# Performance work log

Measured on AMD Instinct MI355X. Metric: run time of the kernel, lower is better.

## Reference

```python
import jax, jax.numpy as jnp
import numpy as np

B, S, H, D = 1, 2048, 24, 128   # batch, img seq, heads, head_dim
RD = 64                          # rotary_emb_dim (partial RoPE)
IPS, IPD = 512, 1152             # ip tokens, ip feature dim
HID = H * D                      # 3072
EPS = 1e-6


def _heads(x):
    # (B, S, H*D) -> (B, H, S, D)
    b, s, _ = x.shape
    return x.reshape(b, s, H, D).transpose(0, 2, 1, 3)


def _rmsnorm(x, scale):
    # RMSNorm with p<0 path: rms = ||x||_2 / sqrt(D); y = scale * x / (rms + eps)
    rms = jnp.linalg.norm(x, axis=-1, keepdims=True) * (D ** -0.5)
    return scale * (x / (rms + EPS))


def _rope(x, sin, cos):
    # rotate-half RoPE on first RD channels, pass-through on the rest
    xr, xp = x[..., :RD], x[..., RD:]
    x1, x2 = jnp.split(xr, 2, axis=-1)
    rot = jnp.concatenate([-x2, x1], axis=-1)
    return jnp.concatenate([xr * cos + rot * sin, xp], axis=-1)


def setup_inputs() -> dict:
    key = jax.random.key(0)
    ks = jax.random.split(key, 16)
    std = 0.02
    inp = {
        "hidden_states": jax.random.normal(ks[0], (B, S, HID), jnp.float32),
        "ip_hidden_states": jax.random.normal(ks[1], (B, IPS, IPD), jnp.float32),
        "sin": jax.random.normal(ks[2], (S, RD), jnp.float32),
        "cos": jax.random.normal(ks[3], (S, RD), jnp.float32),
        "Wq": jax.random.normal(ks[4], (HID, HID), jnp.float32) * std,
        "bq": jnp.zeros((HID,), jnp.float32),
        "Wk": jax.random.normal(ks[5], (HID, HID), jnp.float32) * std,
        "bk": jnp.zeros((HID,), jnp.float32),
        "Wv": jax.random.normal(ks[6], (HID, HID), jnp.float32) * std,
        "bv": jnp.zeros((HID,), jnp.float32),
        "Wo": jax.random.normal(ks[7], (HID, HID), jnp.float32) * std,
        "bo": jnp.zeros((HID,), jnp.float32),
        "Wk_ip": jax.random.normal(ks[8], (HID, IPD), jnp.float32) * std,
        "bk_ip": jnp.zeros((HID,), jnp.float32),
        "Wv_ip": jax.random.normal(ks[9], (HID, IPD), jnp.float32) * std,
        "bv_ip": jnp.zeros((HID,), jnp.float32),
        "q_scale": jnp.ones((D,), jnp.float32),
        "k_scale": jnp.ones((D,), jnp.float32),
    }
    return inp


def reference(hidden_states, ip_hidden_states, sin, cos,
              Wq, bq, Wk, bk, Wv, bv, Wo, bo,
              Wk_ip, bk_ip, Wv_ip, bv_ip, q_scale, k_scale):
    scale = 1.0  # default `scale` kwarg
    # projections (self-attention: encoder_hidden_states = hidden_states)
    q = _heads(hidden_states @ Wq.T + bq)        # (B,H,S,D)
    k = _heads(hidden_states @ Wk.T + bk)
    v = _heads(hidden_states @ Wv.T + bv)
    k_ip = _heads(ip_hidden_states @ Wk_ip.T + bk_ip)   # (B,H,IPS,D)
    v_ip = _heads(ip_hidden_states @ Wv_ip.T + bv_ip)

    # IP branch uses RMS-normed, head_dim^-0.5-scaled, UNROTATED q and k_ip
    # (key_ip is rotated in the source but the rotated value is never used)
    q_norm = _rmsnorm(q, q_scale) * (D ** -0.5)
    k_ip_norm = _rmsnorm(k_ip, k_scale) * (D ** -0.5)

    # main branch: RoPE'd q/k, raw dot product (alpha=1.0, no 1/sqrt(d))
    q_rot = _rope(q, sin, cos)
    k_rot = _rope(k, sin, cos)

    scores = jnp.einsum('bhsd,bhtd->bhst', q_rot, k_rot)
    probs = jax.nn.softmax(scores, axis=-1)
    scores_ip = scale * jnp.einsum('bhsd,bhtd->bhst', q_norm, k_ip_norm)
    probs_ip = jax.nn.softmax(scores_ip, axis=-1)

    out = jnp.einsum('bhst,bhtd->bhsd', probs, v) \
        + jnp.einsum('bhst,bhtd->bhsd', probs_ip, v_ip)
    out = out.transpose(0, 2, 1, 3).reshape(B, S, HID)  # batch_to_head_dim
    out = out @ Wo.T + bo                                # to_out[0]; dropout = id
    return out
```

## Files before the change

kernel.cpp:

```cpp
#include <hip/hip_runtime.h>
#include <stdint.h>

#define S_LEN 2048
#define NH    24
#define HD    128
#define HID   3072
#define IPS   512
#define IPD   1152

using f16   = __fp16;
using f16x4 = __fp16 __attribute__((ext_vector_type(4)));
using f16x8 = __fp16 __attribute__((ext_vector_type(8)));
using f32x4 = float  __attribute__((ext_vector_type(4)));
using f32x16 = float __attribute__((ext_vector_type(16)));

__device__ __forceinline__ void glds16(const f16* g, f16* l) {
  __builtin_amdgcn_global_load_lds((const __attribute__((address_space(1))) void*)g,
                                   (__attribute__((address_space(3))) void*)l,
                                   16, 0, 0);
}

struct CastArgs { const float* src[8]; f16* dst[8]; long n4[8]; };

__global__ void k_cvt_all(CastArgs a, long total4) {
  long i = blockIdx.x * 256L + threadIdx.x;
  if (i >= total4) return;
  long r = i; int s = 0;
  while (r >= a.n4[s]) { r -= a.n4[s]; s++; }
  float4 v = ((const float4*)a.src[s])[r];
  f16x4 o;
  o.x = (f16)v.x; o.y = (f16)v.y; o.z = (f16)v.z; o.w = (f16)v.w;
  ((f16x4*)a.dst[s])[r] = o;
}

__global__ __launch_bounds__(256) void k_gemm_nt(
    const f16* __restrict__ A,
    const f16* __restrict__ B0, const f16* __restrict__ B1, const f16* __restrict__ B2,
    const float* __restrict__ bias0, const float* __restrict__ bias1, const float* __restrict__ bias2,
    void* __restrict__ C0, void* __restrict__ C1, void* __restrict__ C2,
    int M, int N, int K, int out_f32)
{
  const int z = blockIdx.z;
  const f16*   B    = (z == 0) ? B0 : (z == 1) ? B1 : B2;
  const float* bias = (z == 0) ? bias0 : (z == 1) ? bias1 : bias2;
  void*        Cv   = (z == 0) ? C0 : (z == 1) ? C1 : C2;

  __shared__ f16 As[128 * 64];
  __shared__ f16 Bs[128 * 64];

  const int tid = threadIdx.x;
  const int w   = tid >> 6, l = tid & 63;
  const int l31 = l & 31, hi = l >> 5;
  const int bm = blockIdx.y * 128, bn = blockIdx.x * 128;
  const int wm = (w >> 1) * 64,    wn = (w & 1) * 64;

  f32x16 acc[2][2] = {};

  const int r0   = w * 32;
  const int srow = l >> 3;
  const int gch  = (l & 7) ^ (srow & 7);
  const f16* Ag = A + (long)(bm + r0 + srow) * K + gch * 8;
  const f16* Bg = B + (long)(bn + r0 + srow) * K + gch * 8;
  f16* lA = &As[r0 * 64];
  f16* lB = &Bs[r0 * 64];
  const long rs8 = 8L * K;

  const int swz = l & 7;

  for (int k0 = 0; k0 < K; k0 += 64) {
#pragma unroll
    for (int g = 0; g < 4; g++) {
      glds16(Ag + g * rs8 + k0, lA + g * 512);
      glds16(Bg + g * rs8 + k0, lB + g * 512);
    }
    __syncthreads();

#pragma unroll
    for (int ks = 0; ks < 4; ks++) {
      const int pos = ((ks * 2 + hi) ^ swz) * 8;
      f16x8 af[2], bf[2];
#pragma unroll
      for (int mi = 0; mi < 2; mi++)
        af[mi] = *(const f16x8*)&As[(wm + mi * 32 + l31) * 64 + pos];
#pragma unroll
      for (int nj = 0; nj < 2; nj++)
        bf[nj] = *(const f16x8*)&Bs[(wn + nj * 32 + l31) * 64 + pos];
#pragma unroll
      for (int mi = 0; mi < 2; mi++)
#pragma unroll
        for (int nj = 0; nj < 2; nj++)
          acc[mi][nj] = __builtin_amdgcn_mfma_f32_32x32x16_f16(af[mi], bf[nj], acc[mi][nj], 0, 0, 0);
    }
    __syncthreads();
  }

#pragma unroll
  for (int mi = 0; mi < 2; mi++)
#pragma unroll
    for (int nj = 0; nj < 2; nj++) {
      const int col = bn + wn + nj * 32 + l31;
      const float bvv = bias[col];
      const int rowb = bm + wm + mi * 32 + 4 * hi;
#pragma unroll
      for (int reg = 0; reg < 16; reg++) {
        const int row = rowb + (reg & 3) + 8 * (reg >> 2);
        float v = acc[mi][nj][reg] + bvv;
        if (out_f32) ((float*)Cv)[(long)row * N + col] = v;
        else         ((f16*)Cv)[(long)row * N + col] = (f16)v;
      }
    }
}

__global__ void k_qprep(const f16* __restrict__ x, const float* __restrict__ snp,
                        const float* __restrict__ csp, const float* __restrict__ scale,
                        f16* __restrict__ qrot, f16* __restrict__ qnorm, int rows) {
  int gw = (blockIdx.x * 256 + threadIdx.x) >> 6;
  int l  = threadIdx.x & 63;
  if (gw >= rows) return;
  long base = (long)gw * HD;
  int s = gw / NH;
  int d = 2 * l;
  float a = (float)x[base + d];
  float b = (float)x[base + d + 1];

  float ss = a * a + b * b;
#pragma unroll
  for (int off = 32; off >= 1; off >>= 1) ss += __shfl_xor(ss, off, 64);
  float rms = sqrtf(ss * (1.0f / HD));
  float inv = 0.08838834764831845f / (rms + 1e-6f);
  qnorm[base + d]     = (f16)(a * scale[d] * inv);
  qnorm[base + d + 1] = (f16)(b * scale[d + 1] * inv);

  float pa = __shfl_xor(a, 16, 64);
  float pb = __shfl_xor(b, 16, 64);
  float ra, rb;
  if (d < 64) {
    float sgn = (d < 32) ? -1.0f : 1.0f;
    ra = a * csp[s * 64 + d]     + sgn * pa * snp[s * 64 + d];
    rb = b * csp[s * 64 + d + 1] + sgn * pb * snp[s * 64 + d + 1];
  } else {
    ra = a; rb = b;
  }
  qrot[base + d]     = (f16)ra;
  qrot[base + d + 1] = (f16)rb;
}

__global__ void k_krope_pack(const f16* __restrict__ src, const float* __restrict__ snp,
                             const float* __restrict__ csp, f16* __restrict__ dst,
                             int T, int nchunk) {
  int i = blockIdx.x * 256 + threadIdx.x;
  if (i >= nchunk) return;
  int d8 = i % 384;
  int t  = i / 384;
  int h  = d8 >> 4;
  int d  = (d8 & 15) * 8;
  f16x8 x = *(const f16x8*)(src + (long)i * 8);
  f16x8 o;
  if (d < 64) {
    f16x8 p = (d < 32) ? *(const f16x8*)(src + (long)i * 8 + 32)
                       : *(const f16x8*)(src + (long)i * 8 - 32);
    float sgn = (d < 32) ? -1.0f : 1.0f;
#pragma unroll
    for (int j = 0; j < 8; j++) {
      float cs = csp[t * 64 + d + j], sn = snp[t * 64 + d + j];
      o[j] = (f16)((float)x[j] * cs + sgn * (float)p[j] * sn);
    }
  } else {
    o = x;
  }
  long off = ((((long)h * (T >> 4) + (t >> 4)) * 4 + (d >> 5)) * 64 + ((d >> 3) & 3) * 16 + (t & 15)) * 8;
  *(f16x8*)(dst + off) = o;
}

__global__ void k_rms_pack(const f16* __restrict__ x, const float* __restrict__ scale,
                           f16* __restrict__ dst, int T, int rows) {
  int gw  = (blockIdx.x * 256 + threadIdx.x) >> 6;
  int l   = threadIdx.x & 63;
  int sub = l >> 4, l16 = l & 15;
  int row = gw * 4 + sub;
  if (row >= rows) return;
  int t = row / NH, h = row - t * NH;
  int d = l16 * 8;
  f16x8 v = *(const f16x8*)(x + (long)row * HD + d);
  float ss = 0.f;
#pragma unroll
  for (int j = 0; j < 8; j++) { float f = (float)v[j]; ss += f * f; }
  ss += __shfl_xor(ss, 1, 64);
  ss += __shfl_xor(ss, 2, 64);
  ss += __shfl_xor(ss, 4, 64);
  ss += __shfl_xor(ss, 8, 64);
  float rms = sqrtf(ss * (1.0f / HD));
  float inv = 0.08838834764831845f / (rms + 1e-6f);
  f16x8 o;
#pragma unroll
  for (int j = 0; j < 8; j++) o[j] = (f16)((float)v[j] * scale[d + j] * inv);
  long off = ((((long)h * (T >> 4) + (t >> 4)) * 4 + (d >> 5)) * 64 + ((d >> 3) & 3) * 16 + (t & 15)) * 8;
  *(f16x8*)(dst + off) = o;
}

__global__ __launch_bounds__(256) void k_vpack(const f16* __restrict__ v, f16* __restrict__ dst, int T) {
  __shared__ f16 Ts[128 * 72];
  int h = blockIdx.y, tb = blockIdx.x, t0 = tb * 64;
  int tid = threadIdx.x;
  int r = tid >> 2, c4 = tid & 3;
#pragma unroll
  for (int cc = 0; cc < 4; cc++) {
    int ch = c4 * 4 + cc;
    f16x8 x = *(const f16x8*)(v + (long)(t0 + r) * HID + h * HD + ch * 8);
#pragma unroll
    for (int j = 0; j < 8; j++)
      Ts[(ch * 8 + j) * 72 + r] = x[j];
  }
  __syncthreads();
  int l16 = tid & 15, jd = (tid >> 4) & 7, ks = tid >> 7;
#pragma unroll
  for (int quad = 0; quad < 4; quad++) {
    f16x8 x = *(const f16x8*)&Ts[(jd * 16 + l16) * 72 + ks * 32 + quad * 8];
    long off = ((((long)h * (T >> 6) + tb) * 2 + ks) * 8 + jd) * 512 + (quad * 16 + l16) * 8;
    *(f16x8*)(dst + off) = x;
  }
}

__global__ __launch_bounds__(256) void k_flash2(
    const f16* __restrict__ Q, const f16* __restrict__ Kp, const f16* __restrict__ Vp,
    f16* __restrict__ Opart, long part_stride, float2* __restrict__ ml, int p0,
    int T, int Tc)
{
  __shared__ f16 Ps[4][32 * 72];

  const int h    = blockIdx.y;
  const int sp   = blockIdx.z;
  const int tid  = threadIdx.x, w = tid >> 6, l = tid & 63;
  const int quad = l >> 4, l16 = l & 15;
  const int qr   = blockIdx.x * 128 + w * 32;
  const int Tt16 = T >> 4, Tt64 = T >> 6;

  f16x8 qf[2][4];
#pragma unroll
  for (int mt = 0; mt < 2; mt++)
#pragma unroll
    for (int kq = 0; kq < 4; kq++)
      qf[mt][kq] = *(const f16x8*)(Q + (long)(qr + mt * 16 + l16) * HID + h * HD + kq * 32 + quad * 8);

  f32x4 o[2][8] = {};
  float m_run[8], l_run[8];
#pragma unroll
  for (int i = 0; i < 8; i++) { m_run[i] = -1e30f; l_run[i] = 0.f; }

  f16* myP = &Ps[w][0];
  const int t_begin = sp * Tc, t_end = t_begin + Tc;

  for (int t0 = t_begin; t0 < t_end; t0 += 64) {
    f32x4 s[2][4] = {};
#pragma unroll
    for (int kq = 0; kq < 4; kq++) {
      f16x8 kf[4];
#pragma unroll
      for (int jn = 0; jn < 4; jn++)
        kf[jn] = *(const f16x8*)(Kp + (((long)(h * Tt16 + (t0 >> 4) + jn) * 4 + kq) * 64 + l) * 8);
#pragma unroll
      for (int mt = 0; mt < 2; mt++)
#pragma unroll
        for (int jn = 0; jn < 4; jn++)
          s[mt][jn] = __builtin_amdgcn_mfma_f32_16x16x32_f16(qf[mt][kq], kf[jn], s[mt][jn], 0, 0, 0);
    }

#pragma unroll
    for (int mt = 0; mt < 2; mt++) {
#pragma unroll
      for (int r = 0; r < 4; r++) {
        float mx = fmaxf(fmaxf(s[mt][0][r], s[mt][1][r]), fmaxf(s[mt][2][r], s[mt][3][r]));
        mx = fmaxf(mx, __shfl_xor(mx, 1, 64));
        mx = fmaxf(mx, __shfl_xor(mx, 2, 64));
        mx = fmaxf(mx, __shfl_xor(mx, 4, 64));
        mx = fmaxf(mx, __shfl_xor(mx, 8, 64));
        const int ri = mt * 4 + r;
        float mn = fmaxf(m_run[ri], mx);
        float al = __expf(m_run[ri] - mn);
        m_run[ri] = mn;
        float p0v = __expf(s[mt][0][r] - mn);
        float p1v = __expf(s[mt][1][r] - mn);
        float p2v = __expf(s[mt][2][r] - mn);
        float p3v = __expf(s[mt][3][r] - mn);
        s[mt][0][r] = p0v; s[mt][1][r] = p1v; s[mt][2][r] = p2v; s[mt][3][r] = p3v;
        l_run[ri] = l_run[ri] * al + (p0v + p1v + p2v + p3v);
#pragma unroll
        for (int jd = 0; jd < 8; jd++) o[mt][jd][r] *= al;
      }
    }

#pragma unroll
    for (int mt = 0; mt < 2; mt++)
#pragma unroll
      for (int jn = 0; jn < 4; jn++)
#pragma unroll
        for (int r = 0; r < 4; r++)
          myP[(mt * 16 + quad * 4 + r) * 72 + jn * 16 + l16] = (f16)s[mt][jn][r];

#pragma unroll
    for (int ks = 0; ks < 2; ks++) {
      f16x8 pf[2];
#pragma unroll
      for (int mt = 0; mt < 2; mt++)
        pf[mt] = *(const f16x8*)&myP[(mt * 16 + l16) * 72 + ks * 32 + quad * 8];
      f16x8 vf[8];
#pragma unroll
      for (int jd = 0; jd < 8; jd++)
        vf[jd] = *(const f16x8*)(Vp + ((((long)(h * Tt64 + (t0 >> 6)) * 2 + ks) * 8 + jd) * 64 + l) * 8);
#pragma unroll
      for (int jd = 0; jd < 8; jd++)
#pragma unroll
        for (int mt = 0; mt < 2; mt++)
          o[mt][jd] = __builtin_amdgcn_mfma_f32_16x16x32_f16(pf[mt], vf[jd], o[mt][jd], 0, 0, 0);
    }
  }

#pragma unroll
  for (int i = 0; i < 8; i++) {
    float v = l_run[i];
    v += __shfl_xor(v, 1, 64);
    v += __shfl_xor(v, 2, 64);
    v += __shfl_xor(v, 4, 64);
    v += __shfl_xor(v, 8, 64);
    l_run[i] = v;
  }

  f16* Od = Opart + (long)sp * part_stride;
#pragma unroll
  for (int mt = 0; mt < 2; mt++)
#pragma unroll
    for (int jd = 0; jd < 8; jd++)
#pragma unroll
      for (int r = 0; r < 4; r++) {
        int row = qr + mt * 16 + quad * 4 + r;
        int col = h * HD + jd * 16 + l16;
        Od[(long)row * HID + col] = (f16)o[mt][jd][r];
      }
  if (l16 == 0) {
#pragma unroll
    for (int mt = 0; mt < 2; mt++)
#pragma unroll
      for (int r = 0; r < 4; r++) {
        int row = qr + mt * 16 + quad * 4 + r;
        float2 v; v.x = m_run[mt * 4 + r]; v.y = l_run[mt * 4 + r];
        ml[((long)(p0 + sp) * NH + h) * S_LEN + row] = v;
      }
  }
}

__global__ void k_combine(const f16* __restrict__ O0, const f16* __restrict__ O1,
                          const f16* __restrict__ O2, const f16* __restrict__ O3,
                          const f16* __restrict__ O4, const f16* __restrict__ O5,
                          const float2* __restrict__ ml, f16* __restrict__ out, int nchunk) {
  int i = blockIdx.x * 256 + threadIdx.x;
  if (i >= nchunk) return;
  int s = i / 384, d8 = i - s * 384, h = d8 >> 4;
  long base = (long)h * S_LEN + s;
  float2 a0 = ml[0 * NH * S_LEN + base];
  float2 a1 = ml[1L * NH * S_LEN + base];
  float2 a2 = ml[2L * NH * S_LEN + base];
  float2 a3 = ml[3L * NH * S_LEN + base];
  float2 a4 = ml[4L * NH * S_LEN + base];
  float2 a5 = ml[5L * NH * S_LEN + base];
  float M1 = fmaxf(fmaxf(a0.x, a1.x), fmaxf(a2.x, a3.x));
  float e0 = __expf(a0.x - M1), e1 = __expf(a1.x - M1), e2 = __expf(a2.x - M1), e3 = __expf(a3.x - M1);
  float L1 = a0.y * e0 + a1.y * e1 + a2.y * e2 + a3.y * e3;
  float w0 = e0 / L1, w1 = e1 / L1, w2 = e2 / L1, w3 = e3 / L1;
  float M2 = fmaxf(a4.x, a5.x);
  float e4 = __expf(a4.x - M2), e5 = __expf(a5.x - M2);
  float L2 = a4.y * e4 + a5.y * e5;
  float w4 = e4 / L2, w5 = e5 / L2;
  f16x8 v0 = ((const f16x8*)O0)[i];
  f16x8 v1 = ((const f16x8*)O1)[i];
  f16x8 v2 = ((const f16x8*)O2)[i];
  f16x8 v3 = ((const f16x8*)O3)[i];
  f16x8 v4 = ((const f16x8*)O4)[i];
  f16x8 v5 = ((const f16x8*)O5)[i];
  f16x8 r;
#pragma unroll
  for (int j = 0; j < 8; j++) {
    float acc = w0 * (float)v0[j] + w1 * (float)v1[j] + w2 * (float)v2[j] + w3 * (float)v3[j]
              + w4 * (float)v4[j] + w5 * (float)v5[j];
    r[j] = (f16)acc;
  }
  ((f16x8*)out)[i] = r;
}

extern "C" void kernel_launch(void* const* d_in, const int* in_sizes, int n_in,
                              void* d_out, int out_size, void* d_ws, size_t ws_size,
                              hipStream_t stream) {
  const float* hs   = (const float*)d_in[0];
  const float* ip   = (const float*)d_in[1];
  const float* snp  = (const float*)d_in[2];
  const float* csp  = (const float*)d_in[3];
  const float* Wq   = (const float*)d_in[4];
  const float* bq   = (const float*)d_in[5];
  const float* Wk   = (const float*)d_in[6];
  const float* bk   = (const float*)d_in[7];
  const float* Wv   = (const float*)d_in[8];
  const float* bv   = (const float*)d_in[9];
  const float* Wo   = (const float*)d_in[10];
  const float* bo   = (const float*)d_in[11];
  const float* Wkip = (const float*)d_in[12];
  const float* bkip = (const float*)d_in[13];
  const float* Wvip = (const float*)d_in[14];
  const float* bvip = (const float*)d_in[15];
  const float* qs   = (const float*)d_in[16];
  const float* ks   = (const float*)d_in[17];
  float* out = (float*)d_out;

  const long n1   = 6291456;
  const long nW   = 9437184;
  const long nip  = 589824;
  const long nWip = 3538944;

  const long o_hs   = 0;
  const long o_Wq   = 6291456;
  const long o_Wk   = 15728640;
  const long o_Wv   = 25165824;
  const long o_Wo   = 34603008;
  const long o_ip   = 44040192;
  const long o_Wkip = 44630016;
  const long o_Wvip = 48168960;
  const long o_q    = 51707904;
  const long o_k    = 57999360;
  const long o_v    = 64290816;
  const long o_kip  = 70582272;
  const long o_vip  = 72155136;
  const long o_qrot = 73728000;
  const long o_qnorm= 80019456;
  const long o_Vpip = 87883776;
  const long o_ml   = 89456640;
  const long o_Kps  = o_hs;
  const long o_Op0  = o_Wq;
  const long o_Op4  = o_Wkip;
  const long o_Op5  = o_q;
  const long o_Vps  = o_k;
  const long o_Kpip = o_kip;
  const long o_attn = o_v;

  f16* WS = (f16*)d_ws;
  auto P = [&](long off) { return WS + off; };
  float2* mlp = (float2*)(WS + o_ml);

  CastArgs ca;
  ca.src[0] = hs;   ca.dst[0] = P(o_hs);   ca.n4[0] = n1 / 4;
  ca.src[1] = ip;   ca.dst[1] = P(o_ip);   ca.n4[1] = nip / 4;
  ca.src[2] = Wq;   ca.dst[2] = P(o_Wq);   ca.n4[2] = nW / 4;
  ca.src[3] = Wk;   ca.dst[3] = P(o_Wk);   ca.n4[3] = nW / 4;
  ca.src[4] = Wv;   ca.dst[4] = P(o_Wv);   ca.n4[4] = nW / 4;
  ca.src[5] = Wo;   ca.dst[5] = P(o_Wo);   ca.n4[5] = nW / 4;
  ca.src[6] = Wkip; ca.dst[6] = P(o_Wkip); ca.n4[6] = nWip / 4;
  ca.src[7] = Wvip; ca.dst[7] = P(o_Wvip); ca.n4[7] = nWip / 4;
  const long total4 = (n1 + nip + 4 * nW + 2 * nWip) / 4;
  k_cvt_all<<<dim3((total4 + 255) / 256), 256, 0, stream>>>(ca, total4);

  k_gemm_nt<<<dim3(24, 16, 3), 256, 0, stream>>>(P(o_hs),
      P(o_Wq), P(o_Wk), P(o_Wv), bq, bk, bv,
      P(o_q), P(o_k), P(o_v), 2048, 3072, 3072, 0);
  k_gemm_nt<<<dim3(24, 4, 2), 256, 0, stream>>>(P(o_ip),
      P(o_Wkip), P(o_Wvip), P(o_Wvip), bkip, bvip, bvip,
      P(o_kip), P(o_vip), P(o_vip), 512, 3072, 1152, 0);

  k_qprep<<<dim3(49152 / 4), 256, 0, stream>>>(P(o_q), snp, csp, qs, P(o_qrot), P(o_qnorm), 49152);
  k_krope_pack<<<dim3(786432 / 256), 256, 0, stream>>>(P(o_k), snp, csp, P(o_Kps), 2048, 786432);
  k_rms_pack<<<dim3(12288 / 16), 256, 0, stream>>>(P(o_kip), ks, P(o_Kpip), 512, 12288);
  k_vpack<<<dim3(32, 24), 256, 0, stream>>>(P(o_v),   P(o_Vps),  2048);
  k_vpack<<<dim3(8, 24),  256, 0, stream>>>(P(o_vip), P(o_Vpip), 512);

  k_flash2<<<dim3(16, 24, 4), 256, 0, stream>>>(P(o_qrot), P(o_Kps), P(o_Vps),
      P(o_Op0), n1, mlp, 0, 2048, 512);
  k_flash2<<<dim3(16, 24, 2), 256, 0, stream>>>(P(o_qnorm), P(o_Kpip), P(o_Vpip),
      P(o_Op4), o_Op5 - o_Op4, mlp, 4, 512, 256);

  k_combine<<<dim3(786432 / 256), 256, 0, stream>>>(
      P(o_Op0), P(o_Op0 + n1), P(o_Op0 + 2 * n1), P(o_Op0 + 3 * n1),
      P(o_Op4), P(o_Op5), mlp, P(o_attn), 786432);

  k_gemm_nt<<<dim3(24, 16, 1), 256, 0, stream>>>(P(o_attn),
      P(o_Wo), P(o_Wo), P(o_Wo), bo, bo, bo,
      out, out, out, 2048, 3072, 3072, 1);
}
```

Baseline: 692.1 us.

## Rewrite GEMM with 256-wide tiles, triple-buffered LDS pipeline and XCD-aware block mapping

```diff
diff --git a/kernel.cpp b/kernel.cpp
--- a/kernel.cpp
+++ b/kernel.cpp
@@ -12,7 +12,6 @@
 using f16x4 = __fp16 __attribute__((ext_vector_type(4)));
 using f16x8 = __fp16 __attribute__((ext_vector_type(8)));
 using f32x4 = float  __attribute__((ext_vector_type(4)));
-using f32x16 = float __attribute__((ext_vector_type(16)));
 
 __device__ __forceinline__ void glds16(const f16* g, f16* l) {
   __builtin_amdgcn_global_load_lds((const __attribute__((address_space(1))) void*)g,
@@ -33,82 +32,114 @@
   ((f16x4*)a.dst[s])[r] = o;
 }
 
-__global__ __launch_bounds__(256) void k_gemm_nt(
+__global__ __launch_bounds__(512, 2) void k_gemm8(
     const f16* __restrict__ A,
     const f16* __restrict__ B0, const f16* __restrict__ B1, const f16* __restrict__ B2,
     const float* __restrict__ bias0, const float* __restrict__ bias1, const float* __restrict__ bias2,
     void* __restrict__ C0, void* __restrict__ C1, void* __restrict__ C2,
-    int M, int N, int K, int out_f32)
+    int M, int K, int out_f32)
 {
-  const int z = blockIdx.z;
-  const f16*   B    = (z == 0) ? B0 : (z == 1) ? B1 : B2;
-  const float* bias = (z == 0) ? bias0 : (z == 1) ? bias1 : bias2;
-  void*        Cv   = (z == 0) ? C0 : (z == 1) ? C1 : C2;
-
-  __shared__ f16 As[128 * 64];
-  __shared__ f16 Bs[128 * 64];
+  __shared__ f16 As[3][128 * 64];
+  __shared__ f16 Bs[3][256 * 64];
+
+  const int nb   = gridDim.x;
+  const int cpx  = nb >> 3;
+  const int lin  = blockIdx.x;
+  const int sbid = (lin & 7) * cpx + (lin >> 3);
+  const int mtiles = M >> 7;
+  const int ntile  = sbid / mtiles;
+  const int mtile  = sbid - ntile * mtiles;
+  const int widx   = ntile / 12;
+  const int ncol   = (ntile - widx * 12) << 8;
+  const int bm     = mtile << 7;
+
+  const f16*   B    = (widx == 0) ? B0 : (widx == 1) ? B1 : B2;
+  const float* bias = (widx == 0) ? bias0 : (widx == 1) ? bias1 : bias2;
+  void*        Cv   = (widx == 0) ? C0 : (widx == 1) ? C1 : C2;
 
   const int tid = threadIdx.x;
-  const int w   = tid >> 6, l = tid & 63;
-  const int l31 = l & 31, hi = l >> 5;
-  const int bm = blockIdx.y * 128, bn = blockIdx.x * 128;
-  const int wm = (w >> 1) * 64,    wn = (w & 1) * 64;
-
-  f32x16 acc[2][2] = {};
-
-  const int r0   = w * 32;
+  const int w = tid >> 6, l = tid & 63;
+  const int wr = w >> 2, wc = w & 3;
+  const int l15 = l & 15, q = l >> 4, sw = l & 7;
   const int srow = l >> 3;
-  const int gch  = (l & 7) ^ (srow & 7);
-  const f16* Ag = A + (long)(bm + r0 + srow) * K + gch * 8;
-  const f16* Bg = B + (long)(bn + r0 + srow) * K + gch * 8;
-  f16* lA = &As[r0 * 64];
-  f16* lB = &Bs[r0 * 64];
-  const long rs8 = 8L * K;
-
-  const int swz = l & 7;
-
-  for (int k0 = 0; k0 < K; k0 += 64) {
-#pragma unroll
-    for (int g = 0; g < 4; g++) {
-      glds16(Ag + g * rs8 + k0, lA + g * 512);
-      glds16(Bg + g * rs8 + k0, lB + g * 512);
-    }
-    __syncthreads();
-
-#pragma unroll
-    for (int ks = 0; ks < 4; ks++) {
-      const int pos = ((ks * 2 + hi) ^ swz) * 8;
-      f16x8 af[2], bf[2];
-#pragma unroll
-      for (int mi = 0; mi < 2; mi++)
-        af[mi] = *(const f16x8*)&As[(wm + mi * 32 + l31) * 64 + pos];
-#pragma unroll
-      for (int nj = 0; nj < 2; nj++)
-        bf[nj] = *(const f16x8*)&Bs[(wn + nj * 32 + l31) * 64 + pos];
-#pragma unroll
-      for (int mi = 0; mi < 2; mi++)
-#pragma unroll
-        for (int nj = 0; nj < 2; nj++)
-          acc[mi][nj] = __builtin_amdgcn_mfma_f32_32x32x16_f16(af[mi], bf[nj], acc[mi][nj], 0, 0, 0);
-    }
-    __syncthreads();
-  }
-
-#pragma unroll
-  for (int mi = 0; mi < 2; mi++)
-#pragma unroll
-    for (int nj = 0; nj < 2; nj++) {
-      const int col = bn + wn + nj * 32 + l31;
-      const float bvv = bias[col];
-      const int rowb = bm + wm + mi * 32 + 4 * hi;
-#pragma unroll
-      for (int reg = 0; reg < 16; reg++) {
-        const int row = rowb + (reg & 3) + 8 * (reg >> 2);
-        float v = acc[mi][nj][reg] + bvv;
-        if (out_f32) ((float*)Cv)[(long)row * N + col] = v;
-        else         ((f16*)Cv)[(long)row * N + col] = (f16)v;
+  const int sch  = (l & 7) ^ (srow & 7);
+
+  const f16* Ag = A + (long)(bm + w * 16 + srow) * K + sch * 8;
+  const f16* Bg = B + (long)(ncol + w * 32 + srow) * K + sch * 8;
+  const int NT = K >> 6;
+
+  f32x4 acc[4][4] = {};
+  f16x8 af[4], bf[4];
+  const int arow0 = wr * 64 + l15;
+  const int brow0 = wc * 64 + l15;
+
+#define STAGE_A(t, b) { const f16* g_ = Ag + (long)(t) * 64;        \
+    glds16(g_,          &As[b][w * 1024]);                          \
+    glds16(g_ + 8 * K,  &As[b][w * 1024 + 512]); }
+#define STAGE_B1(t, b) { glds16(Bg + (long)(t) * 64, &Bs[b][w * 2048]); }
+#define STAGE_B3(t, b) { const f16* g_ = Bg + (long)(t) * 64;       \
+    glds16(g_ + 8 * K,  &Bs[b][w * 2048 + 512]);                    \
+    glds16(g_ + 16 * K, &Bs[b][w * 2048 + 1024]);                   \
+    glds16(g_ + 24 * K, &Bs[b][w * 2048 + 1536]); }
+#define DSREAD(cb, kq) { const int ck = (((kq) * 4 + q) ^ sw) * 8;  \
+    _Pragma("unroll") for (int mi = 0; mi < 4; mi++)                \
+      af[mi] = *(const f16x8*)&As[cb][(arow0 + mi * 16) * 64 + ck]; \
+    _Pragma("unroll") for (int nj = 0; nj < 4; nj++)                \
+      bf[nj] = *(const f16x8*)&Bs[cb][(brow0 + nj * 16) * 64 + ck]; }
+#define MFMAS() { __builtin_amdgcn_s_setprio(1);                    \
+    _Pragma("unroll") for (int mi = 0; mi < 4; mi++)                \
+    _Pragma("unroll") for (int nj = 0; nj < 4; nj++)                \
+      acc[mi][nj] = __builtin_amdgcn_mfma_f32_16x16x32_f16(af[mi], bf[nj], acc[mi][nj], 0, 0, 0); \
+    __builtin_amdgcn_s_setprio(0); }
+#define ITER(t, cb, pb) {                                           \
+    DSREAD(cb, 0);                                                  \
+    if ((t) + 2 < NT) { STAGE_A((t) + 2, pb); STAGE_B1((t) + 2, pb); } \
+    __builtin_amdgcn_s_barrier();                                   \
+    MFMAS();                                                        \
+    __builtin_amdgcn_s_barrier();                                   \
+    DSREAD(cb, 1);                                                  \
+    if ((t) + 2 < NT) { STAGE_B3((t) + 2, pb);                      \
+      asm volatile("s_waitcnt vmcnt(6)" ::: "memory");              \
+    } else if ((t) + 1 < NT) {                                      \
+      asm volatile("s_waitcnt vmcnt(0)" ::: "memory");              \
+    }                                                               \
+    __builtin_amdgcn_s_barrier();                                   \
+    MFMAS();                                                        \
+    __builtin_amdgcn_s_barrier(); }
+
+  STAGE_A(0, 0); STAGE_B1(0, 0); STAGE_B3(0, 0);
+  STAGE_A(1, 1); STAGE_B1(1, 1); STAGE_B3(1, 1);
+  asm volatile("s_waitcnt vmcnt(6)" ::: "memory");
+  __builtin_amdgcn_s_barrier();
+
+  for (int t = 0; t < NT; t += 3) {
+    ITER(t,     0, 2);
+    ITER(t + 1, 1, 0);
+    ITER(t + 2, 2, 1);
+  }
+
+#undef ITER
+#undef MFMAS
+#undef DSREAD
+#undef STAGE_B3
+#undef STAGE_B1
+#undef STAGE_A
+
+#pragma unroll
+  for (int nj = 0; nj < 4; nj++) {
+    const int col = ncol + wc * 64 + nj * 16 + l15;
+    const float bv_ = bias[col];
+#pragma unroll
+    for (int mi = 0; mi < 4; mi++) {
+      const int row0 = bm + wr * 64 + mi * 16 + q * 4;
+#pragma unroll
+      for (int r = 0; r < 4; r++) {
+        float val = acc[mi][nj][r] + bv_;
+        if (out_f32) ((float*)Cv)[(long)(row0 + r) * HID + col] = val;
+        else         ((f16*)Cv)[(long)(row0 + r) * HID + col] = (f16)val;
       }
     }
+  }
 }
 
 __global__ void k_qprep(const f16* __restrict__ x, const float* __restrict__ snp,
@@ -455,12 +486,12 @@
   const long total4 = (n1 + nip + 4 * nW + 2 * nWip) / 4;
   k_cvt_all<<<dim3((total4 + 255) / 256), 256, 0, stream>>>(ca, total4);
 
-  k_gemm_nt<<<dim3(24, 16, 3), 256, 0, stream>>>(P(o_hs),
+  k_gemm8<<<dim3(576), 512, 0, stream>>>(P(o_hs),
       P(o_Wq), P(o_Wk), P(o_Wv), bq, bk, bv,
-      P(o_q), P(o_k), P(o_v), 2048, 3072, 3072, 0);
-  k_gemm_nt<<<dim3(24, 4, 2), 256, 0, stream>>>(P(o_ip),
+      P(o_q), P(o_k), P(o_v), 2048, 3072, 0);
+  k_gemm8<<<dim3(96), 512, 0, stream>>>(P(o_ip),
       P(o_Wkip), P(o_Wvip), P(o_Wvip), bkip, bvip, bvip,
-      P(o_kip), P(o_vip), P(o_vip), 512, 3072, 1152, 0);
+      P(o_kip), P(o_vip), P(o_vip), 512, 1152, 0);
 
   k_qprep<<<dim3(49152 / 4), 256, 0, stream>>>(P(o_q), snp, csp, qs, P(o_qrot), P(o_qnorm), 49152);
   k_krope_pack<<<dim3(786432 / 256), 256, 0, stream>>>(P(o_k), snp, csp, P(o_Kps), 2048, 786432);
@@ -477,7 +508,7 @@
       P(o_Op0), P(o_Op0 + n1), P(o_Op0 + 2 * n1), P(o_Op0 + 3 * n1),
       P(o_Op4), P(o_Op5), mlp, P(o_attn), 786432);
 
-  k_gemm_nt<<<dim3(24, 16, 1), 256, 0, stream>>>(P(o_attn),
+  k_gemm8<<<dim3(192), 512, 0, stream>>>(P(o_attn),
       P(o_Wo), P(o_Wo), P(o_Wo), bo, bo, bo,
-      out, out, out, 2048, 3072, 3072, 1);
-}
+      out, out, out, 2048, 3072, 1);
+}
```

Result: slower. 706.8 us (+2.1%).

## Fuse K RoPE and packing into QKV GEMM epilogue, merge projection launches, lazy softmax rescale

Applied to the files above, without the earlier changes.

```diff
diff --git a/kernel.cpp b/kernel.cpp
--- a/kernel.cpp
+++ b/kernel.cpp
@@ -33,17 +33,25 @@
   ((f16x4*)a.dst[s])[r] = o;
 }
 
-__global__ __launch_bounds__(256) void k_gemm_nt(
-    const f16* __restrict__ A,
-    const f16* __restrict__ B0, const f16* __restrict__ B1, const f16* __restrict__ B2,
-    const float* __restrict__ bias0, const float* __restrict__ bias1, const float* __restrict__ bias2,
-    void* __restrict__ C0, void* __restrict__ C1, void* __restrict__ C2,
-    int M, int N, int K, int out_f32)
-{
+struct ProjArgs {
+  const f16 *A0, *A1;
+  const f16 *Wq, *Wk, *Wv, *Wkip, *Wvip;
+  const float *bq, *bk, *bv, *bkip, *bvip;
+  f16 *q, *Kps, *v, *kip, *vip;
+  const float *snp, *csp;
+};
+
+__global__ __launch_bounds__(256) void k_gemm_proj(ProjArgs pa) {
   const int z = blockIdx.z;
-  const f16*   B    = (z == 0) ? B0 : (z == 1) ? B1 : B2;
-  const float* bias = (z == 0) ? bias0 : (z == 1) ? bias1 : bias2;
-  void*        Cv   = (z == 0) ? C0 : (z == 1) ? C1 : C2;
+  const f16* A; const f16* B; const float* bias; f16* C; int K;
+  bool rope = false;
+  if (z == 0)      { A = pa.A0; B = pa.Wq;   bias = pa.bq;   C = pa.q;   K = 3072; }
+  else if (z == 1) { A = pa.A0; B = pa.Wk;   bias = pa.bk;   C = pa.Kps; K = 3072; rope = true; }
+  else if (z == 2) { A = pa.A0; B = pa.Wv;   bias = pa.bv;   C = pa.v;   K = 3072; }
+  else if (z == 3) { if (blockIdx.y >= 4) return;
+                     A = pa.A1; B = pa.Wkip; bias = pa.bkip; C = pa.kip; K = 1152; }
+  else             { if (blockIdx.y >= 4) return;
+                     A = pa.A1; B = pa.Wvip; bias = pa.bvip; C = pa.vip; K = 1152; }
 
   __shared__ f16 As[128 * 64];
   __shared__ f16 Bs[128 * 64];
@@ -94,6 +102,118 @@
     __syncthreads();
   }
 
+  if (!rope) {
+#pragma unroll
+    for (int mi = 0; mi < 2; mi++)
+#pragma unroll
+      for (int nj = 0; nj < 2; nj++) {
+        const int col = bn + wn + nj * 32 + l31;
+        const float bvv = bias[col];
+        const int rowb = bm + wm + mi * 32 + 4 * hi;
+#pragma unroll
+        for (int reg = 0; reg < 16; reg++) {
+          const int row = rowb + (reg & 3) + 8 * (reg >> 2);
+          C[(long)row * HID + col] = (f16)(acc[mi][nj][reg] + bvv);
+        }
+      }
+  } else {
+    const int hh = bn >> 7;
+    if (wn == 0) {
+      const float b0 = bias[bn + l31];
+      const float b1 = bias[bn + 32 + l31];
+#pragma unroll
+      for (int mi = 0; mi < 2; mi++) {
+        const int rowb = bm + wm + mi * 32 + 4 * hi;
+#pragma unroll
+        for (int reg = 0; reg < 16; reg++) {
+          const int t = rowb + (reg & 3) + 8 * (reg >> 2);
+          float va = acc[mi][0][reg] + b0;
+          float vb = acc[mi][1][reg] + b1;
+          float cs0 = pa.csp[t * 64 + l31],      sn0 = pa.snp[t * 64 + l31];
+          float cs1 = pa.csp[t * 64 + 32 + l31], sn1 = pa.snp[t * 64 + 32 + l31];
+          float oa = va * cs0 - vb * sn0;
+          float ob = vb * cs1 + va * sn1;
+          const long base = ((long)hh * 128 + (t >> 4)) * 4;
+          const long sub  = (long)(l31 >> 3) * 16 + (t & 15);
+          C[(base + 0) * 512 + sub * 8 + (l31 & 7)] = (f16)oa;
+          C[(base + 1) * 512 + sub * 8 + (l31 & 7)] = (f16)ob;
+        }
+      }
+    } else {
+#pragma unroll
+      for (int nj = 0; nj < 2; nj++) {
+        const int d = 64 + nj * 32 + l31;
+        const float bvv = bias[bn + d];
+#pragma unroll
+        for (int mi = 0; mi < 2; mi++) {
+          const int rowb = bm + wm + mi * 32 + 4 * hi;
+#pragma unroll
+          for (int reg = 0; reg < 16; reg++) {
+            const int t = rowb + (reg & 3) + 8 * (reg >> 2);
+            float v = acc[mi][nj][reg] + bvv;
+            const long off = ((((long)hh * 128 + (t >> 4)) * 4 + (d >> 5)) * 64
+                              + ((d >> 3) & 3) * 16 + (t & 15)) * 8 + (d & 7);
+            C[off] = (f16)v;
+          }
+        }
+      }
+    }
+  }
+}
+
+__global__ __launch_bounds__(256) void k_gemm_nt(
+    const f16* __restrict__ A, const f16* __restrict__ B,
+    const float* __restrict__ bias, float* __restrict__ Cv,
+    int M, int N, int K)
+{
+  __shared__ f16 As[128 * 64];
+  __shared__ f16 Bs[128 * 64];
+
+  const int tid = threadIdx.x;
+  const int w   = tid >> 6, l = tid & 63;
+  const int l31 = l & 31, hi = l >> 5;
+  const int bm = blockIdx.y * 128, bn = blockIdx.x * 128;
+  const int wm = (w >> 1) * 64,    wn = (w & 1) * 64;
+
+  f32x16 acc[2][2] = {};
+
+  const int r0   = w * 32;
+  const int srow = l >> 3;
+  const int gch  = (l & 7) ^ (srow & 7);
+  const f16* Ag = A + (long)(bm + r0 + srow) * K + gch * 8;
+  const f16* Bg = B + (long)(bn + r0 + srow) * K + gch * 8;
+  f16* lA = &As[r0 * 64];
+  f16* lB = &Bs[r0 * 64];
+  const long rs8 = 8L * K;
+  const int swz = l & 7;
+
+  for (int k0 = 0; k0 < K; k0 += 64) {
+#pragma unroll
+    for (int g = 0; g < 4; g++) {
+      glds16(Ag + g * rs8 + k0, lA + g * 512);
+      glds16(Bg + g * rs8 + k0, lB + g * 512);
+    }
+    __syncthreads();
+
+#pragma unroll
+    for (int ks = 0; ks < 4; ks++) {
+      const int pos = ((ks * 2 + hi) ^ swz) * 8;
+      f16x8 af[2], bf[2];
+#pragma unroll
+      for (int mi = 0; mi < 2; mi++)
+        af[mi] = *(const f16x8*)&As[(wm + mi * 32 + l31) * 64 + pos];
+#pragma unroll
+      for (int nj = 0; nj < 2; nj++)
+        bf[nj] = *(const f16x8*)&Bs[(wn + nj * 32 + l31) * 64 + pos];
+#pragma unroll
+      for (int mi = 0; mi < 2; mi++)
+#pragma unroll
+        for (int nj = 0; nj < 2; nj++)
+          acc[mi][nj] = __builtin_amdgcn_mfma_f32_32x32x16_f16(af[mi], bf[nj], acc[mi][nj], 0, 0, 0);
+    }
+    __syncthreads();
+  }
+
 #pragma unroll
   for (int mi = 0; mi < 2; mi++)
 #pragma unroll
@@ -104,9 +224,7 @@
 #pragma unroll
       for (int reg = 0; reg < 16; reg++) {
         const int row = rowb + (reg & 3) + 8 * (reg >> 2);
-        float v = acc[mi][nj][reg] + bvv;
-        if (out_f32) ((float*)Cv)[(long)row * N + col] = v;
-        else         ((f16*)Cv)[(long)row * N + col] = (f16)v;
+        Cv[(long)row * N + col] = acc[mi][nj][reg] + bvv;
       }
     }
 }
@@ -145,33 +263,6 @@
   qrot[base + d + 1] = (f16)rb;
 }
 
-__global__ void k_krope_pack(const f16* __restrict__ src, const float* __restrict__ snp,
-                             const float* __restrict__ csp, f16* __restrict__ dst,
-                             int T, int nchunk) {
-  int i = blockIdx.x * 256 + threadIdx.x;
-  if (i >= nchunk) return;
-  int d8 = i % 384;
-  int t  = i / 384;
-  int h  = d8 >> 4;
-  int d  = (d8 & 15) * 8;
-  f16x8 x = *(const f16x8*)(src + (long)i * 8);
-  f16x8 o;
-  if (d < 64) {
-    f16x8 p = (d < 32) ? *(const f16x8*)(src + (long)i * 8 + 32)
-                       : *(const f16x8*)(src + (long)i * 8 - 32);
-    float sgn = (d < 32) ? -1.0f : 1.0f;
-#pragma unroll
-    for (int j = 0; j < 8; j++) {
-      float cs = csp[t * 64 + d + j], sn = snp[t * 64 + d + j];
-      o[j] = (f16)((float)x[j] * cs + sgn * (float)p[j] * sn);
-    }
-  } else {
-    o = x;
-  }
-  long off = ((((long)h * (T >> 4) + (t >> 4)) * 4 + (d >> 5)) * 64 + ((d >> 3) & 3) * 16 + (t & 15)) * 8;
-  *(f16x8*)(dst + off) = o;
-}
-
 __global__ void k_rms_pack(const f16* __restrict__ x, const float* __restrict__ scale,
                            f16* __restrict__ dst, int T, int rows) {
   int gw  = (blockIdx.x * 256 + threadIdx.x) >> 6;
@@ -265,28 +356,56 @@
           s[mt][jn] = __builtin_amdgcn_mfma_f32_16x16x32_f16(qf[mt][kq], kf[jn], s[mt][jn], 0, 0, 0);
     }
 
-#pragma unroll
-    for (int mt = 0; mt < 2; mt++) {
+    float mx[2][4];
+#pragma unroll
+    for (int mt = 0; mt < 2; mt++)
 #pragma unroll
       for (int r = 0; r < 4; r++) {
-        float mx = fmaxf(fmaxf(s[mt][0][r], s[mt][1][r]), fmaxf(s[mt][2][r], s[mt][3][r]));
-        mx = fmaxf(mx, __shfl_xor(mx, 1, 64));
-        mx = fmaxf(mx, __shfl_xor(mx, 2, 64));
-        mx = fmaxf(mx, __shfl_xor(mx, 4, 64));
-        mx = fmaxf(mx, __shfl_xor(mx, 8, 64));
-        const int ri = mt * 4 + r;
-        float mn = fmaxf(m_run[ri], mx);
-        float al = __expf(m_run[ri] - mn);
-        m_run[ri] = mn;
-        float p0v = __expf(s[mt][0][r] - mn);
-        float p1v = __expf(s[mt][1][r] - mn);
-        float p2v = __expf(s[mt][2][r] - mn);
-        float p3v = __expf(s[mt][3][r] - mn);
-        s[mt][0][r] = p0v; s[mt][1][r] = p1v; s[mt][2][r] = p2v; s[mt][3][r] = p3v;
-        l_run[ri] = l_run[ri] * al + (p0v + p1v + p2v + p3v);
-#pragma unroll
-        for (int jd = 0; jd < 8; jd++) o[mt][jd][r] *= al;
+        float m0 = fmaxf(fmaxf(s[mt][0][r], s[mt][1][r]), fmaxf(s[mt][2][r], s[mt][3][r]));
+        m0 = fmaxf(m0, __shfl_xor(m0, 1, 64));
+        m0 = fmaxf(m0, __shfl_xor(m0, 2, 64));
+        m0 = fmaxf(m0, __shfl_xor(m0, 4, 64));
+        m0 = fmaxf(m0, __shfl_xor(m0, 8, 64));
+        mx[mt][r] = m0;
       }
+    int dfr = 1;
+#pragma unroll
+    for (int mt = 0; mt < 2; mt++)
+#pragma unroll
+      for (int r = 0; r < 4; r++)
+        dfr &= (mx[mt][r] - m_run[mt * 4 + r] <= 8.0f) ? 1 : 0;
+
+    if (__all(dfr)) {
+#pragma unroll
+      for (int mt = 0; mt < 2; mt++)
+#pragma unroll
+        for (int r = 0; r < 4; r++) {
+          const int ri = mt * 4 + r;
+          float p0v = __expf(s[mt][0][r] - m_run[ri]);
+          float p1v = __expf(s[mt][1][r] - m_run[ri]);
+          float p2v = __expf(s[mt][2][r] - m_run[ri]);
+          float p3v = __expf(s[mt][3][r] - m_run[ri]);
+          s[mt][0][r] = p0v; s[mt][1][r] = p1v; s[mt][2][r] = p2v; s[mt][3][r] = p3v;
+          l_run[ri] += p0v + p1v + p2v + p3v;
+        }
+    } else {
+#pragma unroll
+      for (int mt = 0; mt < 2; mt++)
+#pragma unroll
+        for (int r = 0; r < 4; r++) {
+          const int ri = mt * 4 + r;
+          float mn = fmaxf(m_run[ri], mx[mt][r]);
+          float al = __expf(m_run[ri] - mn);
+          m_run[ri] = mn;
+          float p0v = __expf(s[mt][0][r] - mn);
+          float p1v = __expf(s[mt][1][r] - mn);
+          float p2v = __expf(s[mt][2][r] - mn);
+          float p3v = __expf(s[mt][3][r] - mn);
+          s[mt][0][r] = p0v; s[mt][1][r] = p1v; s[mt][2][r] = p2v; s[mt][3][r] = p3v;
+          l_run[ri] = l_run[ri] * al + (p0v + p1v + p2v + p3v);
+#pragma unroll
+          for (int jd = 0; jd < 8; jd++) o[mt][jd][r] *= al;
+        }
     }
 
 #pragma unroll
@@ -431,11 +550,11 @@
   const long o_qnorm= 80019456;
   const long o_Vpip = 87883776;
   const long o_ml   = 89456640;
-  const long o_Kps  = o_hs;
+  const long o_Kps  = o_k;
+  const long o_Vps  = o_hs;
   const long o_Op0  = o_Wq;
   const long o_Op4  = o_Wkip;
   const long o_Op5  = o_q;
-  const long o_Vps  = o_k;
   const long o_Kpip = o_kip;
   const long o_attn = o_v;
 
@@ -455,15 +574,17 @@
   const long total4 = (n1 + nip + 4 * nW + 2 * nWip) / 4;
   k_cvt_all<<<dim3((total4 + 255) / 256), 256, 0, stream>>>(ca, total4);
 
-  k_gemm_nt<<<dim3(24, 16, 3), 256, 0, stream>>>(P(o_hs),
-      P(o_Wq), P(o_Wk), P(o_Wv), bq, bk, bv,
-      P(o_q), P(o_k), P(o_v), 2048, 3072, 3072, 0);
-  k_gemm_nt<<<dim3(24, 4, 2), 256, 0, stream>>>(P(o_ip),
-      P(o_Wkip), P(o_Wvip), P(o_Wvip), bkip, bvip, bvip,
-      P(o_kip), P(o_vip), P(o_vip), 512, 3072, 1152, 0);
+  ProjArgs pa;
+  pa.A0 = P(o_hs); pa.A1 = P(o_ip);
+  pa.Wq = P(o_Wq); pa.Wk = P(o_Wk); pa.Wv = P(o_Wv);
+  pa.Wkip = P(o_Wkip); pa.Wvip = P(o_Wvip);
+  pa.bq = bq; pa.bk = bk; pa.bv = bv; pa.bkip = bkip; pa.bvip = bvip;
+  pa.q = P(o_q); pa.Kps = P(o_Kps); pa.v = P(o_v);
+  pa.kip = P(o_kip); pa.vip = P(o_vip);
+  pa.snp = snp; pa.csp = csp;
+  k_gemm_proj<<<dim3(24, 16, 5), 256, 0, stream>>>(pa);
 
   k_qprep<<<dim3(49152 / 4), 256, 0, stream>>>(P(o_q), snp, csp, qs, P(o_qrot), P(o_qnorm), 49152);
-  k_krope_pack<<<dim3(786432 / 256), 256, 0, stream>>>(P(o_k), snp, csp, P(o_Kps), 2048, 786432);
   k_rms_pack<<<dim3(12288 / 16), 256, 0, stream>>>(P(o_kip), ks, P(o_Kpip), 512, 12288);
   k_vpack<<<dim3(32, 24), 256, 0, stream>>>(P(o_v),   P(o_Vps),  2048);
   k_vpack<<<dim3(8, 24),  256, 0, stream>>>(P(o_vip), P(o_Vpip), 512);
@@ -478,6 +599,5 @@
       P(o_Op4), P(o_Op5), mlp, P(o_attn), 786432);
 
   k_gemm_nt<<<dim3(24, 16, 1), 256, 0, stream>>>(P(o_attn),
-      P(o_Wo), P(o_Wo), P(o_Wo), bo, bo, bo,
-      out, out, out, 2048, 3072, 3072, 1);
-}
+      P(o_Wo), bo, out, 2048, 3072, 3072);
+}
```

Measured after the change: 810.8 us. 17.2% more time.
